# Kernel tuning notes

Hardware: AMD Instinct MI355X
Metric: run time of the kernel (lower is better)

Reference implementation:

```python
import math
import jax, jax.numpy as jnp
import numpy as np

NUM_PRE_NMS = 2000
NMS_THR = 0.7
MIN_SIZE = 16.0
LOG_MAX = math.log(1000.0 / 16)  # clamp on dh, dw as in the torch module

B, A, H, W = 8, 3, 200, 304
STRIDE = 4


def _make_anchors():
    # grid anchors, channel-last anchor ordering to match permute(0,2,3,1)
    sizes = np.array([32.0, 64.0, 128.0], dtype=np.float32)  # A sizes
    ys = (np.arange(H, dtype=np.float32) + 0.5) * STRIDE
    xs = (np.arange(W, dtype=np.float32) + 0.5) * STRIDE
    cy, cx = np.meshgrid(ys, xs, indexing="ij")  # [H,W]
    cx = cx[:, :, None]
    cy = cy[:, :, None]
    half = (sizes / 2.0)[None, None, :]  # [1,1,A]
    anc = np.stack([cx - half, cy - half, cx + half, cy + half], axis=-1)  # [H,W,A,4]
    anc = anc.reshape(-1, 4)  # [H*W*A, 4]
    anc = np.broadcast_to(anc[None], (B, anc.shape[0], 4)).copy()
    return jnp.asarray(anc)


def setup_inputs() -> dict:
    key = jax.random.key(0)
    k1, k2 = jax.random.split(key)
    cls_logits = jax.random.normal(k1, (B, A, H, W), dtype=jnp.float32)
    regs = jax.random.normal(k2, (B, 4 * A, H, W), dtype=jnp.float32) * 0.1
    anchors = _make_anchors()
    return {"cls_logits": cls_logits, "regs": regs, "anchors": anchors,
            "image_h": 800, "image_w": 1216}


def _box_iou(boxes):
    # boxes: [K,4] -> iou [K,K]
    x1, y1, x2, y2 = boxes[:, 0], boxes[:, 1], boxes[:, 2], boxes[:, 3]
    area = (x2 - x1) * (y2 - y1)
    ix1 = jnp.maximum(x1[:, None], x1[None, :])
    iy1 = jnp.maximum(y1[:, None], y1[None, :])
    ix2 = jnp.minimum(x2[:, None], x2[None, :])
    iy2 = jnp.minimum(y2[:, None], y2[None, :])
    iw = jnp.clip(ix2 - ix1, 0.0)
    ih = jnp.clip(iy2 - iy1, 0.0)
    inter = iw * ih
    union = area[:, None] + area[None, :] - inter
    return inter / jnp.maximum(union, 1e-6)


def _nms_one(boxes, valid):
    # boxes sorted by descending score; greedy suppression, fixed-size keep mask
    k = boxes.shape[0]
    iou = _box_iou(boxes)
    later = jnp.arange(k)

    def body(i, keep):
        sup = (iou[i] > NMS_THR) & keep[i] & (later > i)
        return keep & ~sup

    return jax.lax.fori_loop(0, k, body, valid)


def reference(cls_logits, regs, anchors, image_h, image_w):
    b = cls_logits.shape[0]
    # scores/regs in channel-last anchor order (matches permute(0,2,3,1))
    scores = jnp.transpose(cls_logits, (0, 2, 3, 1)).reshape(b, -1)       # [B,N]
    deltas = jnp.transpose(regs, (0, 2, 3, 1)).reshape(b, -1, 4)          # [B,N,4]
    n = scores.shape[1]
    k = min(NUM_PRE_NMS, n)

    top_scores, idx = jax.lax.top_k(scores, k)                            # [B,K]
    top_deltas = jnp.take_along_axis(deltas, idx[:, :, None], axis=1)     # [B,K,4]
    top_anchors = jnp.take_along_axis(anchors, idx[:, :, None], axis=1)   # [B,K,4]

    dx, dy = top_deltas[..., 0], top_deltas[..., 1]
    dh = jnp.minimum(top_deltas[..., 2], LOG_MAX)
    dw = jnp.minimum(top_deltas[..., 3], LOG_MAX)
    ah = top_anchors[..., 3] - top_anchors[..., 1]
    aw = top_anchors[..., 2] - top_anchors[..., 0]
    cx = aw / 2
    cy = ah / 2
    px = cx + dx * aw
    py = cy + dy * ah
    ph = jnp.exp(dh) * ah
    pw = jnp.exp(dw) * aw
    boxes = jnp.stack([px - pw / 2, py - ph / 2, px + pw / 2, py + ph / 2], axis=-1)  # [B,K,4]

    # size filter on clamped coords (as in _nms)
    w_img = jnp.float32(image_w)
    h_img = jnp.float32(image_h)
    bw = jnp.clip(boxes[..., 2], 0.0, w_img) - jnp.clip(boxes[..., 0], 0.0, w_img)
    bh = jnp.clip(boxes[..., 3], 0.0, h_img) - jnp.clip(boxes[..., 1], 0.0, h_img)
    valid = (bw >= MIN_SIZE) & (bh >= MIN_SIZE)

    keep = jax.vmap(_nms_one)(boxes, valid)                               # [B,K]
    out_boxes = boxes * keep[..., None].astype(boxes.dtype)
    return out_boxes, top_scores, keep
```

## Files before the change

kernel.cpp:

```cpp
#include <hip/hip_runtime.h>

#define HWSZ 60800
#define NA 3
#define NTOT 182400
#define KSEL 2000
#define CANDCAP 8192
#define SELCAP 4096
#define NBATCH 8
#define GSPLIT 128
#define LOG_MAX_F 4.135166556742356f

#define OFF_H1    0
#define OFF_CCNT  65536
#define OFF_SCNT  65568
#define ZR_BYTES  65600
#define OFF_SEL   65600
#define OFF_BOX   65728
#define OFF_VALID 321728
#define OFF_SUP   385728
#define OFF_CAND  385728
#define OFF_SELK  910016

__device__ __forceinline__ unsigned int xform(float f) {
    unsigned int b = __float_as_uint(f);
    return b ^ ((unsigned int)((int)b >> 31) | 0x80000000u);
}

__global__ __launch_bounds__(256) void k_hist1(const float* __restrict__ cls,
                                               unsigned int* __restrict__ hist1) {
    int b = blockIdx.y, part = blockIdx.x, tid = threadIdx.x;
    __shared__ unsigned int h[2048];
    for (int i = tid; i < 2048; i += 256) h[i] = 0u;
    __syncthreads();
    const float4* base4 = (const float4*)(cls + (size_t)b * NTOT);
    const int n4 = NTOT / 4;
    int per = (n4 + GSPLIT - 1) / GSPLIT;
    int lo = part * per, hi = lo + per;
    if (hi > n4) hi = n4;
    for (int i = lo + tid; i < hi; i += 256) {
        float4 v = base4[i];
        atomicAdd(&h[xform(v.x) >> 21], 1u);
        atomicAdd(&h[xform(v.y) >> 21], 1u);
        atomicAdd(&h[xform(v.z) >> 21], 1u);
        atomicAdd(&h[xform(v.w) >> 21], 1u);
    }
    __syncthreads();
    unsigned int* gh = hist1 + b * 2048;
    for (int i = tid; i < 2048; i += 256)
        if (h[i]) atomicAdd(&gh[i], h[i]);
}

__global__ __launch_bounds__(1024) void k_scan1(const unsigned int* __restrict__ hist1,
                                                uint4* __restrict__ selinfo) {
    int b = blockIdx.x, tid = threadIdx.x;
    __shared__ unsigned int sa[2048], sb[2048];
    const unsigned int* h = hist1 + b * 2048;
    sa[tid] = h[tid];
    sa[tid + 1024] = h[tid + 1024];
    unsigned int* src = sa; unsigned int* dst = sb;
    for (int d = 1; d < 2048; d <<= 1) {
        __syncthreads();
        dst[tid] = src[tid] + ((tid + d < 2048) ? src[tid + d] : 0u);
        int i2 = tid + 1024;
        dst[i2] = src[i2] + ((i2 + d < 2048) ? src[i2 + d] : 0u);
        unsigned int* t = src; src = dst; dst = t;
    }
    __syncthreads();
    #pragma unroll
    for (int k = 0; k < 2; ++k) {
        int i = tid + k * 1024;
        unsigned int c = src[i];
        unsigned int cn = (i < 2047) ? src[i + 1] : 0u;
        if (c >= KSEL && cn < KSEL)
            selinfo[b] = make_uint4((unsigned int)i, cn, KSEL - cn, 0u);
    }
}

__global__ __launch_bounds__(256) void k_gather(const float* __restrict__ cls,
                                                const uint4* __restrict__ selinfo,
                                                unsigned long long* __restrict__ cand,
                                                unsigned int* __restrict__ ccnt) {
    int b = blockIdx.y, part = blockIdx.x, tid = threadIdx.x;
    unsigned int bin = selinfo[b].x;
    __shared__ unsigned long long lbuf[1024];
    __shared__ unsigned int lcnt, gbase;
    if (tid == 0) lcnt = 0u;
    __syncthreads();
    const float4* base4 = (const float4*)(cls + (size_t)b * NTOT);
    const int n4 = NTOT / 4;
    int per = (n4 + GSPLIT - 1) / GSPLIT;
    int lo = part * per, hi = lo + per;
    if (hi > n4) hi = n4;
    for (int i = lo + tid; i < hi; i += 256) {
        float4 v = base4[i];
        float vals[4] = {v.x, v.y, v.z, v.w};
        int idx0 = i * 4;
        #pragma unroll
        for (int q = 0; q < 4; ++q) {
            unsigned int u = xform(vals[q]);
            if ((u >> 21) >= bin) {
                int idx = idx0 + q;
                int a = idx / HWSZ;
                int hw = idx - a * HWSZ;
                unsigned int n = (unsigned int)(hw * NA + a);
                unsigned int pos = atomicAdd(&lcnt, 1u);
                if (pos < 1024u)
                    lbuf[pos] = ((unsigned long long)u << 32) | (unsigned long long)(~n);
            }
        }
    }
    __syncthreads();
    if (tid == 0) {
        unsigned int c = lcnt < 1024u ? lcnt : 1024u;
        gbase = atomicAdd(&ccnt[b], c);
    }
    __syncthreads();
    unsigned int c = lcnt < 1024u ? lcnt : 1024u;
    unsigned int gb = gbase;
    for (unsigned int i = tid; i < c; i += 256) {
        unsigned int p = gb + i;
        if (p < CANDCAP) cand[(size_t)b * CANDCAP + p] = lbuf[i];
    }
}

__global__ __launch_bounds__(1024) void k_refine(const unsigned long long* __restrict__ cand,
                                                 const unsigned int* __restrict__ ccnt,
                                                 const uint4* __restrict__ selinfo,
                                                 unsigned long long* __restrict__ selk,
                                                 unsigned int* __restrict__ scnt) {
    int b = blockIdx.x;
    int tid = threadIdx.x;
    __shared__ unsigned int sa[2048], sb[2048];
    __shared__ unsigned int acnt, shT;
    uint4 si = selinfo[b];
    unsigned int bin = si.x, krem = si.z;
    unsigned int m = ccnt[b];
    if (m > CANDCAP) m = CANDCAP;
    const unsigned long long* cb = cand + (size_t)b * CANDCAP;

    sa[tid] = 0u; sa[tid + 1024] = 0u;
    if (tid == 0) acnt = 0u;
    __syncthreads();
    for (unsigned int i = tid; i < m; i += 1024) {
        unsigned int u = (unsigned int)(cb[i] >> 32);
        if ((u >> 21) == bin) atomicAdd(&sa[(u >> 10) & 2047u], 1u);
    }
    unsigned int* src = sa; unsigned int* dst = sb;
    for (int d = 1; d < 2048; d <<= 1) {
        __syncthreads();
        dst[tid] = src[tid] + ((tid + d < 2048) ? src[tid + d] : 0u);
        int i2 = tid + 1024;
        dst[i2] = src[i2] + ((i2 + d < 2048) ? src[i2 + d] : 0u);
        unsigned int* t = src; src = dst; dst = t;
    }
    __syncthreads();
    #pragma unroll
    for (int k = 0; k < 2; ++k) {
        int i = tid + k * 1024;
        unsigned int c = src[i];
        unsigned int cn = (i < 2047) ? src[i + 1] : 0u;
        if (c >= krem && cn < krem)
            shT = (bin << 21) | ((unsigned int)i << 10);
    }
    __syncthreads();
    unsigned int T = shT;

    int lane = tid & 63;
    unsigned long long lmask = (1ULL << lane) - 1ULL;
    unsigned int mr = (m + 1023u) & ~1023u;
    unsigned long long* sout = selk + (size_t)b * SELCAP;
    for (unsigned int i = tid; i < mr; i += 1024) {
        bool pred = false;
        unsigned long long key = 0ULL;
        if (i < m) {
            key = cb[i];
            pred = ((unsigned int)(key >> 32)) >= T;
        }
        unsigned long long mask = __ballot(pred);
        unsigned int cw = (unsigned int)__popcll(mask);
        unsigned int base = 0u;
        if (lane == 0 && cw) base = atomicAdd(&acnt, cw);
        base = __shfl(base, 0, 64);
        if (pred) {
            unsigned int pos = base + (unsigned int)__popcll(mask & lmask);
            if (pos < SELCAP) sout[pos] = key;
        }
    }
    __syncthreads();
    if (tid == 0) scnt[b] = (acnt < SELCAP) ? acnt : SELCAP;
}

__global__ __launch_bounds__(256) void k_rank_decode(
        const unsigned long long* __restrict__ selk,
        const unsigned int* __restrict__ scnt,
        const float* __restrict__ regs,
        const float* __restrict__ anchors,
        const int* __restrict__ img_h,
        const int* __restrict__ img_w,
        float* __restrict__ out_scores,
        float4* __restrict__ boxes_ws,
        unsigned int* __restrict__ valid_ws) {
    int b = blockIdx.y;
    int tid = threadIdx.x;
    unsigned int sc = scnt[b];
    if (sc > SELCAP) sc = SELCAP;
    unsigned int kbase = blockIdx.x * 64;
    if (kbase >= sc) return;
    int ki = tid & 63;
    int q = tid >> 6;
    int lane = tid & 63;
    const unsigned long long* sb_ = selk + (size_t)b * SELCAP;
    unsigned int r = kbase + (unsigned int)ki;
    unsigned long long mykey = (r < sc) ? sb_[r] : 0ULL;

    unsigned int qs = ((sc + 255u) >> 8) << 6;
    unsigned int lo = (unsigned int)q * qs;
    unsigned int hi = lo + qs;
    if (hi > sc) hi = sc;

    unsigned int cnt = 0u;
    for (unsigned int base = lo; base < hi; base += 64) {
        unsigned long long kj = 0ULL;
        if (base + (unsigned int)lane < hi) kj = sb_[base + lane];
        unsigned int klo = (unsigned int)kj;
        unsigned int khi = (unsigned int)(kj >> 32);
        #pragma unroll
        for (int t = 0; t < 64; ++t) {
            unsigned int lo_ = (unsigned int)__builtin_amdgcn_readlane((int)klo, t);
            unsigned int hi_ = (unsigned int)__builtin_amdgcn_readlane((int)khi, t);
            unsigned long long kt = ((unsigned long long)hi_ << 32) | (unsigned long long)lo_;
            cnt += (kt > mykey) ? 1u : 0u;
        }
    }
    __shared__ unsigned int cntsh[4][64];
    cntsh[q][ki] = cnt;
    __syncthreads();
    if (tid >= 64) return;
    unsigned int rank = cntsh[0][ki] + cntsh[1][ki] + cntsh[2][ki] + cntsh[3][ki];
    if (r >= sc || rank >= KSEL) return;

    int hv = img_h[0];
    int wv = img_w[0];
    float himg = (hv > 0 && hv < 100000) ? (float)hv : __int_as_float(hv);
    float wimg = (wv > 0 && wv < 100000) ? (float)wv : __int_as_float(wv);

    unsigned int u = (unsigned int)(mykey >> 32);
    unsigned int n = ~((unsigned int)mykey);
    unsigned int bits = (u & 0x80000000u) ? (u & 0x7FFFFFFFu) : ~u;
    float score = __uint_as_float(bits);
    int a = (int)(n % NA);
    int hw = (int)(n / NA);
    const float* rp = regs + ((size_t)b * (4 * NA) + 4 * a) * HWSZ + hw;
    float dx = rp[0 * HWSZ];
    float dy = rp[1 * HWSZ];
    float dh = rp[2 * HWSZ];
    float dw = rp[3 * HWSZ];
    const float* ap = anchors + ((size_t)b * NTOT + n) * 4;
    float ax1 = ap[0], ay1 = ap[1], ax2 = ap[2], ay2 = ap[3];
    float ahh = ay2 - ay1;
    float aww = ax2 - ax1;
    float cx = aww * 0.5f;
    float cy = ahh * 0.5f;
    float px = cx + dx * aww;
    float py = cy + dy * ahh;
    dh = fminf(dh, LOG_MAX_F);
    dw = fminf(dw, LOG_MAX_F);
    float ph = expf(dh) * ahh;
    float pw = expf(dw) * aww;
    float x1 = px - pw * 0.5f;
    float y1 = py - ph * 0.5f;
    float x2 = px + pw * 0.5f;
    float y2 = py + ph * 0.5f;
    float bwv = fminf(fmaxf(x2, 0.f), wimg) - fminf(fmaxf(x1, 0.f), wimg);
    float bhv = fminf(fmaxf(y2, 0.f), himg) - fminf(fmaxf(y1, 0.f), himg);
    unsigned int valid = (bwv >= 16.f && bhv >= 16.f) ? 1u : 0u;
    size_t o = (size_t)b * KSEL + rank;
    out_scores[o] = score;
    boxes_ws[o] = make_float4(x1, y1, x2, y2);
    valid_ws[o] = valid;
}

__global__ __launch_bounds__(256) void k_supmat(const float4* __restrict__ boxes_ws,
                                                unsigned long long* __restrict__ sup) {
    int ct = blockIdx.x;
    int rt = blockIdx.y;
    int b  = blockIdx.z;
    int tid = threadIdx.x;
    __shared__ float4 colbox[64];
    int j0 = ct * 64;
    if (tid < 64) {
        int jl = j0 + tid;
        colbox[tid] = (jl < KSEL) ? boxes_ws[(size_t)b * KSEL + jl]
                                  : make_float4(0.f, 0.f, 0.f, 0.f);
    }
    __syncthreads();
    int i = rt * 256 + tid;
    if (i >= KSEL) return;
    float4 bi = boxes_ws[(size_t)b * KSEL + i];
    float area_i = (bi.z - bi.x) * (bi.w - bi.y);
    unsigned long long word = 0ULL;
    #pragma unroll 8
    for (int jj = 0; jj < 64; ++jj) {
        int j = j0 + jj;
        float4 bj = colbox[jj];
        float area_j = (bj.z - bj.x) * (bj.w - bj.y);
        float ix1 = fmaxf(bi.x, bj.x);
        float iy1 = fmaxf(bi.y, bj.y);
        float ix2 = fminf(bi.z, bj.z);
        float iy2 = fminf(bi.w, bj.w);
        float iw = fmaxf(ix2 - ix1, 0.f);
        float ih = fmaxf(iy2 - iy1, 0.f);
        float inter = iw * ih;
        float uni = area_i + area_j - inter;
        float iou = inter / fmaxf(uni, 1e-6f);
        bool s = (j > i) && (j < KSEL) && (iou > 0.7f);
        if (s) word |= (1ULL << jj);
    }
    sup[((size_t)b * KSEL + i) * 32 + ct] = word;
}

#define LOAD_TILE(wnext, buf)                                                \
    {                                                                        \
        int gbase_ = (wnext) * 2048;                                         \
        _Pragma("unroll")                                                    \
        for (int k = 0; k < 8; ++k) {                                        \
            int e_ = tid + k * 256;                                          \
            int row_ = (wnext) * 64 + (e_ >> 5);                             \
            buf[k] = (row_ < KSEL) ? srow[gbase_ + e_] : 0ULL;               \
        }                                                                    \
    }

#define PROCESS_TILE(w, buf)                                                 \
    {                                                                        \
        if (myword == (w)) {                                                 \
            _Pragma("unroll")                                                \
            for (int k = 0; k < 8; ++k)                                      \
                diag[(tid >> 5) + k * 8] = buf[k];                           \
        }                                                                    \
        __syncthreads();      \
        unsigned long long dval_ = diag[lane];                               \
        unsigned long long nz_ = __ballot(dval_ != 0ULL);                    \
        unsigned int dlo_ = (unsigned int)dval_;                             \
        unsigned int dhi_ = (unsigned int)(dval_ >> 32);                     \
        unsigned long long pend_ =                                           \
            ((unsigned long long)accw[(w) * 2 + 1] << 32)                    \
            | (unsigned long long)accw[(w) * 2];                             \
        unsigned long long c64_ = kws[w] & ~pend_;                           \
        unsigned int clo_ = __builtin_amdgcn_readfirstlane((unsigned int)c64_);        \
        unsigned int chi_ = __builtin_amdgcn_readfirstlane((unsigned int)(c64_ >> 32));\
        unsigned long long cur_ = ((unsigned long long)chi_ << 32)           \
                                  | (unsigned long long)clo_;                \
        if (cur_) {                                                          \
             \
            unsigned long long rem_ = cur_ & nz_;                            \
            while (rem_) {                                                   \
                int bit_ = __builtin_ctzll(rem_);                            \
                unsigned int lo_ = (unsigned int)__builtin_amdgcn_readlane((int)dlo_, bit_); \
                unsigned int hi_ = (unsigned int)__builtin_amdgcn_readlane((int)dhi_, bit_); \
                unsigned long long d_ = ((unsigned long long)hi_ << 32)      \
                                        | (unsigned long long)lo_;           \
                cur_ &= ~d_;                                                 \
                rem_ = cur_ & nz_ & ~((2ULL << bit_) - 1ULL);                \
            }                                                                \
            if (tid == 0) fin[w] = cur_;                                     \
            unsigned long long v_ = 0ULL;                                    \
            _Pragma("unroll")                                                \
            for (int k = 0; k < 8; ++k) {                                    \
                int row_ = (tid >> 5) + k * 8;                               \
                if ((cur_ >> row_) & 1ULL) v_ |= buf[k];                     \
            }                                                                \
            v_ |= __shfl_xor(v_, 32, 64);                                    \
            if (lane < 32 && v_) {                                           \
                atomicOr(&accw[myword * 2], (unsigned int)v_);               \
                atomicOr(&accw[myword * 2 + 1], (unsigned int)(v_ >> 32));   \
            }                                                                \
        } else if (tid == 0) {                                               \
            fin[w] = 0ULL;                                                   \
        }                                                                    \
    }

__global__ __launch_bounds__(256) void k_nms_scan(const unsigned long long* __restrict__ sup,
                                                  const unsigned int* __restrict__ valid_ws,
                                                  const float4* __restrict__ boxes_ws,
                                                  float* __restrict__ out_boxes,
                                                  float* __restrict__ out_keep) {
    int b = blockIdx.x;
    int tid = threadIdx.x;
    int lane = tid & 63;
    int myword = tid & 31;
    __shared__ unsigned long long kws[32];
    __shared__ unsigned long long fin[32];
    __shared__ unsigned long long diag[64];
    __shared__ unsigned int accw[64];
    const unsigned long long* srow = sup + (size_t)b * KSEL * 32;

    if (tid < 32) {
        unsigned long long kw = 0ULL;
        const uint4* vv = (const uint4*)(valid_ws + (size_t)b * KSEL);
        #pragma unroll 4
        for (int q = 0; q < 16; ++q) {
            uint4 x = vv[tid * 16 + q];
            int base = q * 4;
            if (x.x) kw |= 1ULL << (base + 0);
            if (x.y) kw |= 1ULL << (base + 1);
            if (x.z) kw |= 1ULL << (base + 2);
            if (x.w) kw |= 1ULL << (base + 3);
        }
        if (tid == 31) kw &= 0xFFFFULL;
        kws[tid] = kw;
    }
    if (tid < 64) accw[tid] = 0u;

    unsigned long long A[8], B[8];
    LOAD_TILE(0, A);
    LOAD_TILE(1, B);

    for (int t = 0; t < 16; ++t) {
        int w = 2 * t;
        PROCESS_TILE(w, A);
        if (w + 2 < 32) LOAD_TILE(w + 2, A);
        PROCESS_TILE(w + 1, B);
        if (w + 3 < 32) LOAD_TILE(w + 3, B);
    }
    __syncthreads();

    for (int r = tid; r < KSEL; r += 256) {
        float kf = (float)((fin[r >> 6] >> (r & 63)) & 1ULL);
        size_t o = (size_t)b * KSEL + r;
        out_keep[o] = kf;
        float4 bx = boxes_ws[o];
        float* ob = out_boxes + o * 4;
        ob[0] = bx.x * kf;
        ob[1] = bx.y * kf;
        ob[2] = bx.z * kf;
        ob[3] = bx.w * kf;
    }
}

extern "C" void kernel_launch(void* const* d_in, const int* in_sizes, int n_in,
                              void* d_out, int out_size, void* d_ws, size_t ws_size,
                              hipStream_t stream) {
    const float* cls     = (const float*)d_in[0];
    const float* regs    = (const float*)d_in[1];
    const float* anchors = (const float*)d_in[2];
    const int*   img_h   = (const int*)d_in[3];
    const int*   img_w   = (const int*)d_in[4];

    float* out = (float*)d_out;
    float* out_boxes  = out;
    float* out_scores = out + 64000;
    float* out_keep   = out + 80000;

    char* ws = (char*)d_ws;
    unsigned int* hist1      = (unsigned int*)(ws + OFF_H1);
    unsigned int* ccnt       = (unsigned int*)(ws + OFF_CCNT);
    unsigned int* scnt       = (unsigned int*)(ws + OFF_SCNT);
    uint4* selinfo           = (uint4*)(ws + OFF_SEL);
    float4* boxes_ws         = (float4*)(ws + OFF_BOX);
    unsigned int* valid_ws   = (unsigned int*)(ws + OFF_VALID);
    unsigned long long* sup  = (unsigned long long*)(ws + OFF_SUP);
    unsigned long long* cand = (unsigned long long*)(ws + OFF_CAND);
    unsigned long long* selk = (unsigned long long*)(ws + OFF_SELK);

    hipMemsetAsync(ws, 0, ZR_BYTES, stream);
    k_hist1<<<dim3(GSPLIT, NBATCH), 256, 0, stream>>>(cls, hist1);
    k_scan1<<<NBATCH, 1024, 0, stream>>>(hist1, selinfo);
    k_gather<<<dim3(GSPLIT, NBATCH), 256, 0, stream>>>(cls, selinfo, cand, ccnt);
    k_refine<<<NBATCH, 1024, 0, stream>>>(cand, ccnt, selinfo, selk, scnt);
    k_rank_decode<<<dim3(SELCAP / 64, NBATCH), 256, 0, stream>>>(selk, scnt, regs, anchors,
                                                                 img_h, img_w, out_scores,
                                                                 boxes_ws, valid_ws);
    k_supmat<<<dim3(32, 8, NBATCH), 256, 0, stream>>>(boxes_ws, sup);
    k_nms_scan<<<NBATCH, 256, 0, stream>>>(sup, valid_ws, boxes_ws, out_boxes, out_keep);
}
```

Baseline: 199.6 us.

## Fuse histogram scan and candidate refine into producer kernels via last-block pattern

```diff
diff --git a/kernel.cpp b/kernel.cpp
--- a/kernel.cpp
+++ b/kernel.cpp
@@ -13,23 +13,29 @@
 #define OFF_H1    0
 #define OFF_CCNT  65536
 #define OFF_SCNT  65568
-#define ZR_BYTES  65600
-#define OFF_SEL   65600
-#define OFF_BOX   65728
-#define OFF_VALID 321728
-#define OFF_SUP   385728
-#define OFF_CAND  385728
-#define OFF_SELK  910016
+#define OFF_DONE1 65600
+#define OFF_DONE2 65632
+#define ZR_BYTES  65664
+#define OFF_SEL   65664
+#define OFF_BOX   65792
+#define OFF_VALID 321792
+#define OFF_SUP   385792
+#define OFF_CAND  385792
+#define OFF_SELK  910080
 
 __device__ __forceinline__ unsigned int xform(float f) {
     unsigned int b = __float_as_uint(f);
     return b ^ ((unsigned int)((int)b >> 31) | 0x80000000u);
 }
 
-__global__ __launch_bounds__(256) void k_hist1(const float* __restrict__ cls,
-                                               unsigned int* __restrict__ hist1) {
+__global__ __launch_bounds__(256) void k_hist_scan(const float* __restrict__ cls,
+                                                   unsigned int* __restrict__ hist1,
+                                                   unsigned int* __restrict__ done1,
+                                                   uint4* __restrict__ selinfo) {
     int b = blockIdx.y, part = blockIdx.x, tid = threadIdx.x;
     __shared__ unsigned int h[2048];
+    __shared__ unsigned int h2[2048];
+    __shared__ int amLast;
     for (int i = tid; i < 2048; i += 256) h[i] = 0u;
     __syncthreads();
     const float4* base4 = (const float4*)(cls + (size_t)b * NTOT);
@@ -48,27 +54,26 @@
     unsigned int* gh = hist1 + b * 2048;
     for (int i = tid; i < 2048; i += 256)
         if (h[i]) atomicAdd(&gh[i], h[i]);
-}
-
-__global__ __launch_bounds__(1024) void k_scan1(const unsigned int* __restrict__ hist1,
-                                                uint4* __restrict__ selinfo) {
-    int b = blockIdx.x, tid = threadIdx.x;
-    __shared__ unsigned int sa[2048], sb[2048];
-    const unsigned int* h = hist1 + b * 2048;
-    sa[tid] = h[tid];
-    sa[tid + 1024] = h[tid + 1024];
-    unsigned int* src = sa; unsigned int* dst = sb;
+    __syncthreads();
+    if (tid == 0) {
+        __threadfence();
+        unsigned int d = atomicAdd(&done1[b], 1u);
+        amLast = (d == GSPLIT - 1) ? 1 : 0;
+    }
+    __syncthreads();
+    if (!amLast) return;
+    __threadfence();
+
+    for (int i = tid; i < 2048; i += 256) h[i] = atomicAdd(&gh[i], 0u);
+    __syncthreads();
+    unsigned int* src = h; unsigned int* dst = h2;
     for (int d = 1; d < 2048; d <<= 1) {
+        for (int i = tid; i < 2048; i += 256)
+            dst[i] = src[i] + ((i + d < 2048) ? src[i + d] : 0u);
+        unsigned int* t = src; src = dst; dst = t;
         __syncthreads();
-        dst[tid] = src[tid] + ((tid + d < 2048) ? src[tid + d] : 0u);
-        int i2 = tid + 1024;
-        dst[i2] = src[i2] + ((i2 + d < 2048) ? src[i2 + d] : 0u);
-        unsigned int* t = src; src = dst; dst = t;
-    }
-    __syncthreads();
-    #pragma unroll
-    for (int k = 0; k < 2; ++k) {
-        int i = tid + k * 1024;
+    }
+    for (int i = tid; i < 2048; i += 256) {
         unsigned int c = src[i];
         unsigned int cn = (i < 2047) ? src[i + 1] : 0u;
         if (c >= KSEL && cn < KSEL)
@@ -76,14 +81,20 @@
     }
 }
 
-__global__ __launch_bounds__(256) void k_gather(const float* __restrict__ cls,
-                                                const uint4* __restrict__ selinfo,
-                                                unsigned long long* __restrict__ cand,
-                                                unsigned int* __restrict__ ccnt) {
+__global__ __launch_bounds__(256) void k_gather_refine(const float* __restrict__ cls,
+                                                       const uint4* __restrict__ selinfo,
+                                                       unsigned long long* __restrict__ cand,
+                                                       unsigned int* __restrict__ ccnt,
+                                                       unsigned int* __restrict__ done2,
+                                                       unsigned long long* __restrict__ selk,
+                                                       unsigned int* __restrict__ scnt) {
     int b = blockIdx.y, part = blockIdx.x, tid = threadIdx.x;
-    unsigned int bin = selinfo[b].x;
+    uint4 si = selinfo[b];
+    unsigned int bin = si.x, krem = si.z;
     __shared__ unsigned long long lbuf[1024];
-    __shared__ unsigned int lcnt, gbase;
+    __shared__ unsigned int sa[2048], sb2[2048];
+    __shared__ unsigned int lcnt, gbase, acnt, shT;
+    __shared__ int amLast;
     if (tid == 0) lcnt = 0u;
     __syncthreads();
     const float4* base4 = (const float4*)(cls + (size_t)b * NTOT);
@@ -121,45 +132,39 @@
         unsigned int p = gb + i;
         if (p < CANDCAP) cand[(size_t)b * CANDCAP + p] = lbuf[i];
     }
-}
-
-__global__ __launch_bounds__(1024) void k_refine(const unsigned long long* __restrict__ cand,
-                                                 const unsigned int* __restrict__ ccnt,
-                                                 const uint4* __restrict__ selinfo,
-                                                 unsigned long long* __restrict__ selk,
-                                                 unsigned int* __restrict__ scnt) {
-    int b = blockIdx.x;
-    int tid = threadIdx.x;
-    __shared__ unsigned int sa[2048], sb[2048];
-    __shared__ unsigned int acnt, shT;
-    uint4 si = selinfo[b];
-    unsigned int bin = si.x, krem = si.z;
-    unsigned int m = ccnt[b];
+    __syncthreads();
+    if (tid == 0) {
+        __threadfence();
+        unsigned int d = atomicAdd(&done2[b], 1u);
+        amLast = (d == GSPLIT - 1) ? 1 : 0;
+    }
+    __syncthreads();
+    if (!amLast) return;
+    __threadfence();
+
+    unsigned int m = atomicAdd(&ccnt[b], 0u);
     if (m > CANDCAP) m = CANDCAP;
     const unsigned long long* cb = cand + (size_t)b * CANDCAP;
 
-    sa[tid] = 0u; sa[tid + 1024] = 0u;
+    for (int i = tid; i < 2048; i += 256) sa[i] = 0u;
     if (tid == 0) acnt = 0u;
     __syncthreads();
-    for (unsigned int i = tid; i < m; i += 1024) {
+    for (unsigned int i = tid; i < m; i += 256) {
         unsigned int u = (unsigned int)(cb[i] >> 32);
         if ((u >> 21) == bin) atomicAdd(&sa[(u >> 10) & 2047u], 1u);
     }
-    unsigned int* src = sa; unsigned int* dst = sb;
+    __syncthreads();
+    unsigned int* src = sa; unsigned int* dst = sb2;
     for (int d = 1; d < 2048; d <<= 1) {
+        for (int i = tid; i < 2048; i += 256)
+            dst[i] = src[i] + ((i + d < 2048) ? src[i + d] : 0u);
+        unsigned int* t = src; src = dst; dst = t;
         __syncthreads();
-        dst[tid] = src[tid] + ((tid + d < 2048) ? src[tid + d] : 0u);
-        int i2 = tid + 1024;
-        dst[i2] = src[i2] + ((i2 + d < 2048) ? src[i2 + d] : 0u);
-        unsigned int* t = src; src = dst; dst = t;
-    }
-    __syncthreads();
-    #pragma unroll
-    for (int k = 0; k < 2; ++k) {
-        int i = tid + k * 1024;
-        unsigned int c = src[i];
+    }
+    for (int i = tid; i < 2048; i += 256) {
+        unsigned int cc = src[i];
         unsigned int cn = (i < 2047) ? src[i + 1] : 0u;
-        if (c >= krem && cn < krem)
+        if (cc >= krem && cn < krem)
             shT = (bin << 21) | ((unsigned int)i << 10);
     }
     __syncthreads();
@@ -167,9 +172,9 @@
 
     int lane = tid & 63;
     unsigned long long lmask = (1ULL << lane) - 1ULL;
-    unsigned int mr = (m + 1023u) & ~1023u;
+    unsigned int mr = (m + 255u) & ~255u;
     unsigned long long* sout = selk + (size_t)b * SELCAP;
-    for (unsigned int i = tid; i < mr; i += 1024) {
+    for (unsigned int i = tid; i < mr; i += 256) {
         bool pred = false;
         unsigned long long key = 0ULL;
         if (i < m) {
@@ -455,6 +460,8 @@
     unsigned int* hist1      = (unsigned int*)(ws + OFF_H1);
     unsigned int* ccnt       = (unsigned int*)(ws + OFF_CCNT);
     unsigned int* scnt       = (unsigned int*)(ws + OFF_SCNT);
+    unsigned int* done1      = (unsigned int*)(ws + OFF_DONE1);
+    unsigned int* done2      = (unsigned int*)(ws + OFF_DONE2);
     uint4* selinfo           = (uint4*)(ws + OFF_SEL);
     float4* boxes_ws         = (float4*)(ws + OFF_BOX);
     unsigned int* valid_ws   = (unsigned int*)(ws + OFF_VALID);
@@ -463,10 +470,9 @@
     unsigned long long* selk = (unsigned long long*)(ws + OFF_SELK);
 
     hipMemsetAsync(ws, 0, ZR_BYTES, stream);
-    k_hist1<<<dim3(GSPLIT, NBATCH), 256, 0, stream>>>(cls, hist1);
-    k_scan1<<<NBATCH, 1024, 0, stream>>>(hist1, selinfo);
-    k_gather<<<dim3(GSPLIT, NBATCH), 256, 0, stream>>>(cls, selinfo, cand, ccnt);
-    k_refine<<<NBATCH, 1024, 0, stream>>>(cand, ccnt, selinfo, selk, scnt);
+    k_hist_scan<<<dim3(GSPLIT, NBATCH), 256, 0, stream>>>(cls, hist1, done1, selinfo);
+    k_gather_refine<<<dim3(GSPLIT, NBATCH), 256, 0, stream>>>(cls, selinfo, cand, ccnt,
+                                                              done2, selk, scnt);
     k_rank_decode<<<dim3(SELCAP / 64, NBATCH), 256, 0, stream>>>(selk, scnt, regs, anchors,
                                                                  img_h, img_w, out_scores,
                                                                  boxes_ws, valid_ws);
```

New measurement: 252.4 us. 1.26x slower.
